# Kernel tuning notes

Measured on AMD Instinct MI355X. Metric: run time of the kernel, lower is better.

The kernel has to match this reference:

```python
import jax, jax.numpy as jnp
import numpy as np

D = 64  # hidden size

def _ffn2(x, w1, b1, w2, b2):
    # Linear -> ReLU -> Linear (no activation after last layer, matching FFN)
    return jax.nn.relu(x @ w1 + b1) @ w2 + b2

def setup_inputs() -> dict:
    key = jax.random.key(0)
    ks = jax.random.split(key, 40)
    B, NP, NY, NO = 512, 128, 1024, 256
    f32 = jnp.float32
    def n(k, sh, s=0.1):
        return (jax.random.normal(k, sh) * s).astype(f32)
    inp = {
        'pred_state': jax.random.normal(ks[0], (B, NP, 2), dtype=f32),
        'prey_state': jax.random.normal(ks[1], (B, NY, 2), dtype=f32),
        'obst_state': jax.random.normal(ks[2], (B, NO, 3), dtype=f32),
        'prey_is_alive': jax.random.randint(ks[3], (B, NY), 0, 2).astype(bool),
        'emb': n(ks[4], (3, D)),
        'e0_w1': n(ks[5], (2, D)), 'e0_b1': n(ks[6], (D,)),
        'e0_w2': n(ks[7], (D, D)), 'e0_b2': n(ks[8], (D,)),
        'e1_w1': n(ks[9], (2, D)), 'e1_b1': n(ks[10], (D,)),
        'e1_w2': n(ks[11], (D, D)), 'e1_b2': n(ks[12], (D,)),
        'e2_w1': n(ks[13], (3, D)), 'e2_b1': n(ks[14], (D,)),
        'e2_w2': n(ks[15], (D, D)), 'e2_b2': n(ks[16], (D,)),
        'wq': n(ks[17], (D, D)), 'bq': n(ks[18], (D,)),
        'wk': n(ks[19], (D, D)), 'bk': n(ks[20], (D,)),
        'wv': n(ks[21], (D, D)), 'bv': n(ks[22], (D,)),
        'wp': n(ks[23], (2, D)), 'bp': n(ks[24], (D,)),
        'wo': n(ks[25], (D, D)), 'bo': n(ks[26], (D,)),
        'n_w1': n(ks[27], (D, D)), 'n_b1': n(ks[28], (D,)),
        'n_w2': n(ks[29], (D, D)), 'n_b2': n(ks[30], (D,)),
        'n_w3': n(ks[31], (D, 1), s=0.01), 'n_b3': n(ks[32], (1,)),
    }
    return inp

def reference(pred_state, prey_state, obst_state, prey_is_alive, emb,
              e0_w1, e0_b1, e0_w2, e0_b2,
              e1_w1, e1_b1, e1_w2, e1_b2,
              e2_w1, e2_b1, e2_w2, e2_b2,
              wq, bq, wk, bk, wv, bv, wp, bp, wo, bo,
              n_w1, n_b1, n_w2, n_b2, n_w3, n_b3):
    # per-entity encoders + type embedding
    x_pred = _ffn2(pred_state, e0_w1, e0_b1, e0_w2, e0_b2) + emb[0]  # [B,NP,D]
    x_prey = _ffn2(prey_state, e1_w1, e1_b1, e1_w2, e1_b2) + emb[1]  # [B,NY,D]
    x_obst = _ffn2(obst_state, e2_w1, e2_b1, e2_w2, e2_b2) + emb[2]  # [B,NO,D]
    x = jnp.concatenate([x_pred, x_prey, x_obst], axis=1)            # [B,N,D]
    pos = jnp.concatenate([pred_state, prey_state, obst_state[..., :2]], axis=1)  # [B,N,2]
    # NOTE: original mask = zeros.unsqueeze(-1) & (...) is identically False -> no masking.
    q = x_pred @ wq + bq   # [B,NP,D]
    k = x @ wk + bk        # [B,N,D]
    v = x @ wv + bv        # [B,N,D]
    # relative positional key bias: pbias = (pos_q - pos_k) @ wp; q . pbias folded as below
    qp = q @ wp.T          # [B,NP,2]
    scale = np.float32(1.0 / np.sqrt(D))
    scores = (jnp.einsum('bqd,bkd->bqk', q, k)
              + jnp.einsum('bqc,bqc->bq', qp, pred_state)[..., None]
              - jnp.einsum('bqc,bkc->bqk', qp, pos)
              + (q @ bp)[..., None]) * scale          # [B,NP,N]
    a = jax.nn.softmax(scores, axis=-1)
    out = jnp.einsum('bqk,bkd->bqd', a, v) @ wo + bo  # [B,NP,D]
    # output FFN with final Tanh
    h = jax.nn.relu(out @ n_w1 + n_b1)
    h = jax.nn.relu(h @ n_w2 + n_b2)
    return jnp.tanh(h @ n_w3 + n_b3)                  # [B,NP,1]
```

## Files before the change

### kernel.cpp

```cpp
#include <hip/hip_runtime.h>
#include <math.h>

#define NB 512
#define NPQ 128
#define NY 1024
#define NO 256
#define NTOT 1408

typedef __attribute__((ext_vector_type(8))) short bf16x8;
typedef __attribute__((ext_vector_type(4))) float f32x4;

__device__ __forceinline__ unsigned short f2bf(float f) {
    unsigned int u = __float_as_uint(f);
    u += 0x7fffu + ((u >> 16) & 1u);
    return (unsigned short)(u >> 16);
}
__device__ __forceinline__ float bf2f(short s) {
    return __uint_as_float(((unsigned int)(unsigned short)s) << 16);
}

union U8  { bf16x8 v; unsigned long long u[2]; };
union U16 { bf16x8 v; uint4 u; };

__global__ __launch_bounds__(256) void k_prep(
    const float* __restrict__ emb,  const float* __restrict__ e0b2,
    const float* __restrict__ e0w2, const float* __restrict__ wq,
    const float* __restrict__ bq,   const float* __restrict__ wk,
    const float* __restrict__ bk,   const float* __restrict__ wp,
    const float* __restrict__ bp,   const float* __restrict__ wvv,
    const float* __restrict__ bv,   const float* __restrict__ wo,
    const float* __restrict__ bo,
    const float* __restrict__ e1b2, const float* __restrict__ e1w2,
    const float* __restrict__ e2b2, const float* __restrict__ e2w2,
    const float* __restrict__ nw1,  const float* __restrict__ nw2,
    float* __restrict__ a0, float* __restrict__ b0g0, float* __restrict__ bvo,
    float* __restrict__ BEP,
    unsigned short* __restrict__ W2P, unsigned short* __restrict__ AqkP,
    unsigned short* __restrict__ P3P, unsigned short* __restrict__ WHP)
{
    const int tid = threadIdx.x;
    __shared__ float sW2q[4096];
    __shared__ float sWvo[4096];
    __shared__ float sAqk[4096];
    __shared__ float sP3[1024];
    __shared__ float scq[64];

    const float* w2s[3] = {e0w2, e1w2, e2w2};
    for (int idx = tid; idx < 1536; idx += 256) {
        const int t = idx >> 9, rem = idx & 511;
        const int mt = rem >> 7, rem2 = rem & 127;
        const int kh = rem2 >> 6, lane = rem2 & 63;
        const int quad = lane >> 4, lq = lane & 15;
        const float* w2 = w2s[t];
        unsigned short v[8];
        #pragma unroll
        for (int j = 0; j < 8; ++j)
            v[j] = f2bf(w2[(kh*32 + quad*8 + j)*64 + mt*16 + lq]);
        *(uint4*)&W2P[(size_t)idx*8] = make_uint4(
            (unsigned int)v[0] | ((unsigned int)v[1] << 16),
            (unsigned int)v[2] | ((unsigned int)v[3] << 16),
            (unsigned int)v[4] | ((unsigned int)v[5] << 16),
            (unsigned int)v[6] | ((unsigned int)v[7] << 16));
    }
    const float* b2s[3] = {e0b2, e1b2, e2b2};
    for (int idx = tid; idx < 192; idx += 256) {
        const int t = idx >> 6, d = idx & 63;
        BEP[idx] = b2s[t][d] + emb[t*64 + d];
    }

    for (int idx = tid; idx < 4096; idx += 256) {
        const int h = idx >> 6, j = idx & 63;
        float s = 0.f;
        for (int e = 0; e < 64; ++e) s += e0w2[h*64+e] * wq[e*64+j];
        sW2q[idx] = s;
    }
    if (tid < 64) {
        const int j = tid;
        float s = bq[j];
        for (int e = 0; e < 64; ++e) s += (e0b2[e] + emb[e]) * wq[e*64+j];
        scq[j] = s;
    }
    for (int idx = tid; idx < 4096; idx += 256) {
        const int e = idx >> 6, o = idx & 63;
        float s = 0.f;
        for (int d = 0; d < 64; ++d) s += wvv[e*64+d] * wo[d*64+o];
        sWvo[idx] = s;
    }
    if (tid < 64) {
        const int o = tid;
        float s = bo[o];
        for (int d = 0; d < 64; ++d) s += bv[d] * wo[d*64+o];
        bvo[o] = s;
    }
    __syncthreads();
    for (int idx = tid; idx < 4096; idx += 256) {
        const int h = idx >> 6, d = idx & 63;
        float s = 0.f;
        for (int j = 0; j < 64; ++j) s += sW2q[h*64+j] * wk[d*64+j];
        sAqk[idx] = s;
    }
    if (tid < 64) {
        const int d = tid;
        float s = 0.f;
        for (int j = 0; j < 64; ++j) s += scq[j] * wk[d*64+j];
        a0[d] = s;
    }
    for (int i = tid; i < 1024; i += 256) {
        const int c = i >> 6, h = i & 63;
        float s = 0.f;
        if (c == 0 || c == 1) {
            for (int j = 0; j < 64; ++j) s += sW2q[h*64+j] * wp[c*64+j];
        } else if (c == 2) {
            for (int j = 0; j < 64; ++j) s += sW2q[h*64+j] * (bp[j] + bk[j]);
        }
        sP3[i] = s;
    }
    if (tid == 0) {
        float s0 = 0.f, s1 = 0.f, s2 = 0.f;
        for (int j = 0; j < 64; ++j) {
            s0 += scq[j] * wp[j];
            s1 += scq[j] * wp[64+j];
            s2 += scq[j] * (bp[j] + bk[j]);
        }
        b0g0[0] = s0; b0g0[1] = s1; b0g0[2] = s2;
    }
    __syncthreads();
    for (int idx = tid; idx < 512; idx += 256) {
        const int fi = idx >> 6, lane = idx & 63;
        const int mt = fi >> 1, kh = fi & 1;
        const int quad = lane >> 4, lq = lane & 15;
        unsigned short v[8];
        #pragma unroll
        for (int j = 0; j < 8; ++j)
            v[j] = f2bf(sAqk[(kh*32 + quad*8 + j)*64 + mt*16 + lq]);
        *(uint4*)&AqkP[(size_t)idx*8] = make_uint4(
            (unsigned int)v[0] | ((unsigned int)v[1] << 16),
            (unsigned int)v[2] | ((unsigned int)v[3] << 16),
            (unsigned int)v[4] | ((unsigned int)v[5] << 16),
            (unsigned int)v[6] | ((unsigned int)v[7] << 16));
    }
    for (int idx = tid; idx < 128; idx += 256) {
        const int kh = idx >> 6, lane = idx & 63;
        const int quad = lane >> 4, lq = lane & 15;
        unsigned short v[8];
        #pragma unroll
        for (int j = 0; j < 8; ++j)
            v[j] = f2bf(sP3[lq*64 + kh*32 + quad*8 + j]);
        *(uint4*)&P3P[(size_t)idx*8] = make_uint4(
            (unsigned int)v[0] | ((unsigned int)v[1] << 16),
            (unsigned int)v[2] | ((unsigned int)v[3] << 16),
            (unsigned int)v[4] | ((unsigned int)v[5] << 16),
            (unsigned int)v[6] | ((unsigned int)v[7] << 16));
    }
    for (int idx = tid; idx < 1536; idx += 256) {
        const int l = idx >> 9, rem = idx & 511;
        const int mt = rem >> 7, rem2 = rem & 127;
        const int kh = rem2 >> 6, lane = rem2 & 63;
        const int quad = lane >> 4, lq = lane & 15;
        unsigned short v[8];
        #pragma unroll
        for (int j = 0; j < 8; ++j) {
            const int off = (kh*32 + quad*8 + j)*64 + mt*16 + lq;
            const float x = (l == 0) ? sWvo[off] : ((l == 1) ? nw1[off] : nw2[off]);
            v[j] = f2bf(x);
        }
        *(uint4*)&WHP[(size_t)idx*8] = make_uint4(
            (unsigned int)v[0] | ((unsigned int)v[1] << 16),
            (unsigned int)v[2] | ((unsigned int)v[3] << 16),
            (unsigned int)v[4] | ((unsigned int)v[5] << 16),
            (unsigned int)v[6] | ((unsigned int)v[7] << 16));
    }
}

__global__ __launch_bounds__(256) void k_encq(
    const float* __restrict__ pred, const float* __restrict__ prey,
    const float* __restrict__ obst,
    const unsigned short* __restrict__ W2P, const float* __restrict__ BEP,
    const float* __restrict__ e0w1, const float* __restrict__ e0b1,
    const float* __restrict__ e1w1, const float* __restrict__ e1b1,
    const float* __restrict__ e2w1, const float* __restrict__ e2b1,
    const unsigned short* __restrict__ AqkP, const float* __restrict__ a0,
    const unsigned short* __restrict__ P3P,  const float* __restrict__ b0g0,
    unsigned short* __restrict__ X, float* __restrict__ POS,
    float* __restrict__ QT, float* __restrict__ QP, float* __restrict__ QC)
{
    const int tid = threadIdx.x, lane = tid & 63, w = tid >> 6;
    const int lq = lane & 15, quad = lane >> 4;
    __shared__ __align__(16) short sH[4][32][68];

    if (blockIdx.x < 1408) {
        const int blk = blockIdx.x;
        int type, lrow0, cin, lsh, nmask, nbase;
        const float *st, *w1, *b1;
        if (blk < 128)       { type=0; lrow0=blk*512;         st=pred; w1=e0w1; b1=e0b1; cin=2; lsh=7;  nmask=NPQ-1; nbase=0; }
        else if (blk < 1152) { type=1; lrow0=(blk-128)*512;   st=prey; w1=e1w1; b1=e1b1; cin=2; lsh=10; nmask=NY-1;  nbase=NPQ; }
        else                 { type=2; lrow0=(blk-1152)*512;  st=obst; w1=e2w1; b1=e2b1; cin=3; lsh=8;  nmask=NO-1;  nbase=NPQ+NY; }

        bf16x8 wfrag[4][2];
        #pragma unroll
        for (int mt = 0; mt < 4; ++mt)
            #pragma unroll
            for (int kh = 0; kh < 2; ++kh)
                wfrag[mt][kh] = *(const bf16x8*)&W2P[(size_t)(((type*4 + mt)*2 + kh)*64 + lane)*8];

        float4 be[4];
        #pragma unroll
        for (int mt = 0; mt < 4; ++mt)
            be[mt] = *(const float4*)&BEP[type*64 + mt*16 + quad*4];

        float b1v[2][8], w0v[2][8], w1v[2][8], w2v[2][8];
        #pragma unroll
        for (int kh = 0; kh < 2; ++kh) {
            const int k0 = kh*32 + quad*8;
            *(float4*)&b1v[kh][0] = *(const float4*)&b1[k0];
            *(float4*)&b1v[kh][4] = *(const float4*)&b1[k0+4];
            *(float4*)&w0v[kh][0] = *(const float4*)&w1[k0];
            *(float4*)&w0v[kh][4] = *(const float4*)&w1[k0+4];
            *(float4*)&w1v[kh][0] = *(const float4*)&w1[64+k0];
            *(float4*)&w1v[kh][4] = *(const float4*)&w1[64+k0+4];
            if (cin == 3) {
                *(float4*)&w2v[kh][0] = *(const float4*)&w1[128+k0];
                *(float4*)&w2v[kh][4] = *(const float4*)&w1[128+k0+4];
            }
        }

        #pragma unroll
        for (int k = 0; k < 4; ++k) {
            const int i = tid*4 + k;
            const int r = i >> 1, c = i & 1;
            const int lr = lrow0 + r;
            const int pb = lr >> lsh, n = nbase + (lr & nmask);
            POS[((size_t)pb*NTOT + n)*2 + c] = st[(size_t)lr*cin + c];
        }

        for (int rt = 0; rt < 8; ++rt) {
            const int lr = lrow0 + w*128 + rt*16 + lq;
            float s0, s1, s2 = 0.f;
            if (cin == 2) {
                const float2 sv = *(const float2*)&st[(size_t)lr*2];
                s0 = sv.x; s1 = sv.y;
            } else {
                const float2 sv = *(const float2*)&st[(size_t)lr*3];
                s0 = sv.x; s1 = sv.y; s2 = st[(size_t)lr*3 + 2];
            }
            bf16x8 hb[2];
            #pragma unroll
            for (int kh = 0; kh < 2; ++kh)
                #pragma unroll
                for (int j = 0; j < 8; ++j) {
                    float a = b1v[kh][j] + s0*w0v[kh][j] + s1*w1v[kh][j];
                    if (cin == 3) a += s2*w2v[kh][j];
                    hb[kh][j] = (short)f2bf(fmaxf(a, 0.f));
                }

            f32x4 acc[4];
            #pragma unroll
            for (int mt = 0; mt < 4; ++mt) acc[mt] = (f32x4){0.f,0.f,0.f,0.f};
            #pragma unroll
            for (int mt = 0; mt < 4; ++mt) {
                acc[mt] = __builtin_amdgcn_mfma_f32_16x16x32_bf16(wfrag[mt][0], hb[0], acc[mt], 0, 0, 0);
                acc[mt] = __builtin_amdgcn_mfma_f32_16x16x32_bf16(wfrag[mt][1], hb[1], acc[mt], 0, 0, 0);
            }

            const int bb = lr >> lsh, n = nbase + (lr & nmask);
            unsigned short* xbase = X + ((size_t)bb*NTOT + n)*64;
            #pragma unroll
            for (int mt = 0; mt < 4; ++mt) {
                const unsigned int u0 = (unsigned int)f2bf(acc[mt][0] + be[mt].x)
                                      | ((unsigned int)f2bf(acc[mt][1] + be[mt].y) << 16);
                const unsigned int u1 = (unsigned int)f2bf(acc[mt][2] + be[mt].z)
                                      | ((unsigned int)f2bf(acc[mt][3] + be[mt].w) << 16);
                *(uint2*)(xbase + mt*16 + quad*4) = make_uint2(u0, u1);
            }
        }
    } else {
        const int b = blockIdx.x - 1408;
        const float w1r0 = e0w1[lane], w1r1 = e0w1[64+lane], b1r = e0b1[lane];
        {
            const float* sp = pred + ((size_t)b*NPQ + w*32)*2;
            #pragma unroll
            for (int r = 0; r < 32; ++r) {
                const float a = b1r + sp[2*r]*w1r0 + sp[2*r+1]*w1r1;
                sH[w][r][lane] = (short)f2bf(fmaxf(a, 0.f));
            }
        }

        bf16x8 wfrag[4][2], a3[2];
        #pragma unroll
        for (int mt = 0; mt < 4; ++mt)
            #pragma unroll
            for (int kh = 0; kh < 2; ++kh)
                wfrag[mt][kh] = *(const bf16x8*)&AqkP[(size_t)((mt*2 + kh)*64 + lane)*8];
        #pragma unroll
        for (int kh = 0; kh < 2; ++kh)
            a3[kh] = *(const bf16x8*)&P3P[(size_t)(kh*64 + lane)*8];

        float4 a0r[4];
        #pragma unroll
        for (int mt = 0; mt < 4; ++mt) a0r[mt] = *(const float4*)&a0[mt*16 + quad*4];
        const float c0 = b0g0[0], c1 = b0g0[1], c2 = b0g0[2];

        __syncthreads();

        for (int bt = 0; bt < 2; ++bt) {
            U8 hb0, hb1;
            const short* hp = &sH[w][bt*16 + lq][0];
            hb0.u[0] = *(const unsigned long long*)(hp + quad*8);
            hb0.u[1] = *(const unsigned long long*)(hp + quad*8 + 4);
            hb1.u[0] = *(const unsigned long long*)(hp + 32 + quad*8);
            hb1.u[1] = *(const unsigned long long*)(hp + 32 + quad*8 + 4);

            f32x4 acc[4], acc3;
            #pragma unroll
            for (int mt = 0; mt < 4; ++mt) acc[mt] = (f32x4){0.f,0.f,0.f,0.f};
            acc3 = (f32x4){0.f,0.f,0.f,0.f};
            #pragma unroll
            for (int mt = 0; mt < 4; ++mt) {
                acc[mt] = __builtin_amdgcn_mfma_f32_16x16x32_bf16(wfrag[mt][0], hb0.v, acc[mt], 0, 0, 0);
                acc[mt] = __builtin_amdgcn_mfma_f32_16x16x32_bf16(wfrag[mt][1], hb1.v, acc[mt], 0, 0, 0);
            }
            acc3 = __builtin_amdgcn_mfma_f32_16x16x32_bf16(a3[0], hb0.v, acc3, 0, 0, 0);
            acc3 = __builtin_amdgcn_mfma_f32_16x16x32_bf16(a3[1], hb1.v, acc3, 0, 0, 0);

            const int row = b*NPQ + w*32 + bt*16 + lq;
            #pragma unroll
            for (int mt = 0; mt < 4; ++mt) {
                *(float4*)&QT[(size_t)row*64 + mt*16 + quad*4] = make_float4(
                    acc[mt][0] + a0r[mt].x, acc[mt][1] + a0r[mt].y,
                    acc[mt][2] + a0r[mt].z, acc[mt][3] + a0r[mt].w);
            }
            if (quad == 0) {
                const float qp0 = acc3[0] + c0, qp1 = acc3[1] + c1, qs = acc3[2] + c2;
                const float p0 = pred[(size_t)row*2], p1 = pred[(size_t)row*2 + 1];
                QP[(size_t)row*2]     = qp0;
                QP[(size_t)row*2 + 1] = qp1;
                QC[row] = qp0*p0 + qp1*p1 + qs;
            }
        }
    }
}

__global__ __launch_bounds__(256, 2) void k_attn(
    const unsigned short* __restrict__ X, const float* __restrict__ POS,
    const float* __restrict__ QT, const float* __restrict__ QP,
    const float* __restrict__ QC, float* __restrict__ OPRE)
{
    const int tid = threadIdx.x, b = blockIdx.x;
    const int w = tid >> 6, lane = tid & 63, lq = lane & 15, quad = lane >> 4;

    __shared__ __align__(16) short sXc[2][64][68];
    __shared__ __align__(16) short sP[4][32][68];

    bf16x8 aq[2][2];
    #pragma unroll
    for (int qt = 0; qt < 2; ++qt) {
        const float* qrow = QT + ((size_t)b*NPQ + w*32 + qt*16 + lq)*64;
        #pragma unroll
        for (int kh = 0; kh < 2; ++kh)
            #pragma unroll
            for (int j = 0; j < 8; ++j)
                aq[qt][kh][j] = (short)f2bf(qrow[kh*32 + quad*8 + j]);
    }

    float qcr[2][4], qp0r[2][4], qp1r[2][4], lacc[2][4];
    f32x4 O[2][4];
    #pragma unroll
    for (int qt = 0; qt < 2; ++qt)
        #pragma unroll
        for (int i = 0; i < 4; ++i) {
            const size_t g = (size_t)b*NPQ + w*32 + qt*16 + quad*4 + i;
            qcr[qt][i]  = QC[g];
            qp0r[qt][i] = -QP[2*g];
            qp1r[qt][i] = -QP[2*g+1];
            lacc[qt][i] = 0.f;
        }
    #pragma unroll
    for (int qt = 0; qt < 2; ++qt)
        #pragma unroll
        for (int nt = 0; nt < 4; ++nt) O[qt][nt] = (f32x4){0.f,0.f,0.f,0.f};
    const float E = 0.180336884f;

    const int skey = tid & 63, sd0 = (tid >> 6) * 16;

    for (int kt = 0; kt < 22; ++kt) {
        const int par = kt & 1;

        const unsigned short* gx = X + ((size_t)b*NTOT + kt*64 + skey)*64 + sd0;
        const uint4 t0 = *(const uint4*)(gx);
        const uint4 t1 = *(const uint4*)(gx + 8);

        if (kt > 0) {
            const int pb = par ^ 1;
            #pragma unroll
            for (int kc = 0; kc < 2; ++kc) {
                U8 pa[2];
                #pragma unroll
                for (int qt = 0; qt < 2; ++qt) {
                    const short* pp = &sP[w][qt*16 + lq][kc*32 + quad*8];
                    pa[qt].u[0] = *(const unsigned long long*)pp;
                    pa[qt].u[1] = *(const unsigned long long*)(pp + 4);
                }
                #pragma unroll
                for (int nt = 0; nt < 4; ++nt) {
                    U8 bv;
                    const short* xp = &sXc[pb][nt*16 + lq][kc*32 + quad*8];
                    bv.u[0] = *(const unsigned long long*)xp;
                    bv.u[1] = *(const unsigned long long*)(xp + 4);
                    O[0][nt] = __builtin_amdgcn_mfma_f32_16x16x32_bf16(pa[0].v, bv.v, O[0][nt], 0, 0, 0);
                    O[1][nt] = __builtin_amdgcn_mfma_f32_16x16x32_bf16(pa[1].v, bv.v, O[1][nt], 0, 0, 0);
                }
            }
        }

        __builtin_amdgcn_sched_barrier(0);

        #pragma unroll
        for (int nt = 0; nt < 4; ++nt) {
            U16 bx0, bx1;
            const unsigned short* xrow = X + ((size_t)b*NTOT + kt*64 + nt*16 + lq)*64;
            bx0.u = *(const uint4*)(xrow + quad*8);
            bx1.u = *(const uint4*)(xrow + 32 + quad*8);
            const float pos0 = POS[((size_t)b*NTOT + kt*64 + nt*16 + lq)*2];
            const float pos1 = POS[((size_t)b*NTOT + kt*64 + nt*16 + lq)*2 + 1];
            #pragma unroll
            for (int qt = 0; qt < 2; ++qt) {
                f32x4 sa = (f32x4){0.f,0.f,0.f,0.f};
                sa = __builtin_amdgcn_mfma_f32_16x16x32_bf16(aq[qt][0], bx0.v, sa, 0, 0, 0);
                sa = __builtin_amdgcn_mfma_f32_16x16x32_bf16(aq[qt][1], bx1.v, sa, 0, 0, 0);
                #pragma unroll
                for (int i = 0; i < 4; ++i) {
                    float s = sa[i] + qcr[qt][i];
                    s = fmaf(qp0r[qt][i], pos0, s);
                    s = fmaf(qp1r[qt][i], pos1, s);
                    const float p = exp2f(s * E);
                    lacc[qt][i] += p;
                    sP[w][qt*16 + quad*4 + i][nt*16 + lq] = (short)f2bf(p);
                }
            }
        }

        {
            unsigned short tmp[16];
            *(uint4*)tmp = t0; *(uint4*)(tmp+8) = t1;
            #pragma unroll
            for (int j = 0; j < 16; ++j) sXc[par][sd0+j][skey] = (short)tmp[j];
        }

        __syncthreads();
    }

    {
        #pragma unroll
        for (int kc = 0; kc < 2; ++kc) {
            U8 pa[2];
            #pragma unroll
            for (int qt = 0; qt < 2; ++qt) {
                const short* pp = &sP[w][qt*16 + lq][kc*32 + quad*8];
                pa[qt].u[0] = *(const unsigned long long*)pp;
                pa[qt].u[1] = *(const unsigned long long*)(pp + 4);
            }
            #pragma unroll
            for (int nt = 0; nt < 4; ++nt) {
                U8 bv;
                const short* xp = &sXc[1][nt*16 + lq][kc*32 + quad*8];
                bv.u[0] = *(const unsigned long long*)xp;
                bv.u[1] = *(const unsigned long long*)(xp + 4);
                O[0][nt] = __builtin_amdgcn_mfma_f32_16x16x32_bf16(pa[0].v, bv.v, O[0][nt], 0, 0, 0);
                O[1][nt] = __builtin_amdgcn_mfma_f32_16x16x32_bf16(pa[1].v, bv.v, O[1][nt], 0, 0, 0);
            }
        }
    }

    #pragma unroll
    for (int qt = 0; qt < 2; ++qt)
        #pragma unroll
        for (int i = 0; i < 4; ++i) {
            #pragma unroll
            for (int off = 1; off < 16; off <<= 1)
                lacc[qt][i] += __shfl_xor(lacc[qt][i], off);
            const float rl = 1.f / lacc[qt][i];
            float* orow = OPRE + ((size_t)b*NPQ + w*32 + qt*16 + quad*4 + i)*64;
            #pragma unroll
            for (int nt = 0; nt < 4; ++nt) orow[nt*16 + lq] = O[qt][nt][i] * rl;
        }
}

__global__ __launch_bounds__(256) void k_head(
    const float* __restrict__ OPRE,
    const unsigned short* __restrict__ WHP,
    const float* __restrict__ bvo, const float* __restrict__ nb1,
    const float* __restrict__ nb2,
    const float* __restrict__ nw3, const float* __restrict__ nb3,
    float* __restrict__ OUT)
{
    const int tid = threadIdx.x, b = blockIdx.x;
    const int w = tid >> 6, lane = tid & 63, lq = lane & 15, quad = lane >> 4;
    __shared__ __align__(16) short sA[128][68];
    __shared__ __align__(16) short sB[128][68];
    __shared__ float sw3[64];

    for (int i = tid*4; i < 8192; i += 1024) {
        const float4 v = *(const float4*)&OPRE[(size_t)b*8192 + i];
        const int r = i >> 6, d = i & 63;
        const unsigned int u0 = (unsigned int)f2bf(v.x) | ((unsigned int)f2bf(v.y) << 16);
        const unsigned int u1 = (unsigned int)f2bf(v.z) | ((unsigned int)f2bf(v.w) << 16);
        *(uint2*)&sA[r][d] = make_uint2(u0, u1);
    }
    if (tid < 64) sw3[tid] = nw3[tid];
    __syncthreads();

    const float* Bs[3] = {bvo, nb1, nb2};
    for (int l = 0; l < 3; ++l) {
        bf16x8 wfrag[4][2];
        #pragma unroll
        for (int mt = 0; mt < 4; ++mt)
            #pragma unroll
            for (int kh = 0; kh < 2; ++kh)
                wfrag[mt][kh] = *(const bf16x8*)&WHP[(size_t)(((l*4 + mt)*2 + kh)*64 + lane)*8];
        const float* Bb = Bs[l];
        float be[4][4];
        #pragma unroll
        for (int mt = 0; mt < 4; ++mt)
            #pragma unroll
            for (int i = 0; i < 4; ++i) be[mt][i] = Bb[mt*16 + quad*4 + i];

        short (*src)[68] = (l & 1) ? sB : sA;
        short (*dst)[68] = (l & 1) ? sA : sB;
        const bool doRelu = (l >= 1);

        for (int bt = 0; bt < 2; ++bt) {
            U8 hb0, hb1;
            const short* hp = &src[w*32 + bt*16 + lq][0];
            hb0.u[0] = *(const unsigned long long*)(hp + quad*8);
            hb0.u[1] = *(const unsigned long long*)(hp + quad*8 + 4);
            hb1.u[0] = *(const unsigned long long*)(hp + 32 + quad*8);
            hb1.u[1] = *(const unsigned long long*)(hp + 32 + quad*8 + 4);

            f32x4 acc[4];
            #pragma unroll
            for (int mt = 0; mt < 4; ++mt) acc[mt] = (f32x4){0.f,0.f,0.f,0.f};
            #pragma unroll
            for (int mt = 0; mt < 4; ++mt) {
                acc[mt] = __builtin_amdgcn_mfma_f32_16x16x32_bf16(wfrag[mt][0], hb0.v, acc[mt], 0, 0, 0);
                acc[mt] = __builtin_amdgcn_mfma_f32_16x16x32_bf16(wfrag[mt][1], hb1.v, acc[mt], 0, 0, 0);
            }
            const int row = w*32 + bt*16 + lq;
            #pragma unroll
            for (int mt = 0; mt < 4; ++mt) {
                float v0 = acc[mt][0] + be[mt][0];
                float v1 = acc[mt][1] + be[mt][1];
                float v2 = acc[mt][2] + be[mt][2];
                float v3 = acc[mt][3] + be[mt][3];
                if (doRelu) {
                    v0 = fmaxf(v0, 0.f); v1 = fmaxf(v1, 0.f);
                    v2 = fmaxf(v2, 0.f); v3 = fmaxf(v3, 0.f);
                }
                const unsigned int u0 = (unsigned int)f2bf(v0) | ((unsigned int)f2bf(v1) << 16);
                const unsigned int u1 = (unsigned int)f2bf(v2) | ((unsigned int)f2bf(v3) << 16);
                *(uint2*)&dst[row][mt*16 + quad*4] = make_uint2(u0, u1);
            }
        }
        __syncthreads();
    }

    if (tid < 128) {
        const int row = tid;
        float acc = nb3[0];
        #pragma unroll 16
        for (int d = 0; d < 64; ++d) acc += bf2f(sB[row][d]) * sw3[d];
        OUT[(size_t)b*NPQ + row] = tanhf(acc);
    }
}

extern "C" void kernel_launch(void* const* d_in, const int* in_sizes, int n_in,
                              void* d_out, int out_size, void* d_ws, size_t ws_size,
                              hipStream_t stream)
{
    const float* pred = (const float*)d_in[0];
    const float* prey = (const float*)d_in[1];
    const float* obst = (const float*)d_in[2];
    const float* emb  = (const float*)d_in[4];
    const float* e0w1 = (const float*)d_in[5];
    const float* e0b1 = (const float*)d_in[6];
    const float* e0w2 = (const float*)d_in[7];
    const float* e0b2 = (const float*)d_in[8];
    const float* e1w1 = (const float*)d_in[9];
    const float* e1b1 = (const float*)d_in[10];
    const float* e1w2 = (const float*)d_in[11];
    const float* e1b2 = (const float*)d_in[12];
    const float* e2w1 = (const float*)d_in[13];
    const float* e2b1 = (const float*)d_in[14];
    const float* e2w2 = (const float*)d_in[15];
    const float* e2b2 = (const float*)d_in[16];
    const float* wq  = (const float*)d_in[17];
    const float* bq  = (const float*)d_in[18];
    const float* wk  = (const float*)d_in[19];
    const float* bk  = (const float*)d_in[20];
    const float* wvv = (const float*)d_in[21];
    const float* bv  = (const float*)d_in[22];
    const float* wp  = (const float*)d_in[23];
    const float* bp  = (const float*)d_in[24];
    const float* wo  = (const float*)d_in[25];
    const float* bo  = (const float*)d_in[26];
    const float* nw1 = (const float*)d_in[27];
    const float* nb1 = (const float*)d_in[28];
    const float* nw2 = (const float*)d_in[29];
    const float* nb2 = (const float*)d_in[30];
    const float* nw3 = (const float*)d_in[31];
    const float* nb3 = (const float*)d_in[32];

    char* ws = (char*)d_ws;
    unsigned short* X = (unsigned short*)ws;
    float* F    = (float*)(ws + 92274688);
    float* POS  = F;
    float* QT   = POS + 1441792;
    float* QP   = QT  + 4194304;
    float* QC   = QP  + 131072;
    float* OPRE = QC  + 65536;
    float* a0   = OPRE + 4194304;
    float* b0g0 = a0  + 64;
    float* bvo  = b0g0 + 4;
    float* BEP  = bvo + 64;
    unsigned short* W2P  = (unsigned short*)(BEP + 192);
    unsigned short* AqkP = W2P + 12288;
    unsigned short* P3P  = AqkP + 4096;
    unsigned short* WHP  = P3P + 1024;

    k_prep<<<1, 256, 0, stream>>>(emb, e0b2, e0w2, wq, bq, wk, bk, wp, bp,
        wvv, bv, wo, bo, e1b2, e1w2, e2b2, e2w2, nw1, nw2,
        a0, b0g0, bvo, BEP, W2P, AqkP, P3P, WHP);
    k_encq<<<1920, 256, 0, stream>>>(pred, prey, obst, W2P, BEP,
        e0w1, e0b1, e1w1, e1b1, e2w1, e2b1,
        AqkP, a0, P3P, b0g0, X, POS, QT, QP, QC);
    k_attn<<<512, 256, 0, stream>>>(X, POS, QT, QP, QC, OPRE);
    k_head<<<512, 256, 0, stream>>>(OPRE, WHP, bvo, nb1, nb2,
        nw3, nb3, (float*)d_out);
}
```

Baseline: 303.7 us.

## Split single-block weight prep kernel into two multi-block kernels

The one-block preprocessing kernel, which folds weight matrices (W2·Wq, Wv·Wo, Aqk, P3) and packs them into bf16 MFMA layouts, is split into two launches. The first runs 43 blocks and the second runs 4, with intermediate fused matrices staged in global workspace instead of shared memory. This spreads the serial 64x64x64 matrix products across many compute units and adds multiple accumulators to shorten dependency chains. It costs one extra kernel launch and a global-memory round trip for the intermediates.

Measured after the change: 256.3 us. 15.6% less time.

```diff
diff --git a/kernel.cpp b/kernel.cpp
--- a/kernel.cpp
+++ b/kernel.cpp
@@ -22,153 +22,216 @@
 union U8  { bf16x8 v; unsigned long long u[2]; };
 union U16 { bf16x8 v; uint4 u; };
 
-__global__ __launch_bounds__(256) void k_prep(
+__global__ __launch_bounds__(256) void k_prepA(
     const float* __restrict__ emb,  const float* __restrict__ e0b2,
     const float* __restrict__ e0w2, const float* __restrict__ wq,
-    const float* __restrict__ bq,   const float* __restrict__ wk,
-    const float* __restrict__ bk,   const float* __restrict__ wp,
-    const float* __restrict__ bp,   const float* __restrict__ wvv,
-    const float* __restrict__ bv,   const float* __restrict__ wo,
-    const float* __restrict__ bo,
+    const float* __restrict__ bq,   const float* __restrict__ wp,
+    const float* __restrict__ bp,   const float* __restrict__ bk,
+    const float* __restrict__ wvv,  const float* __restrict__ bv,
+    const float* __restrict__ wo,   const float* __restrict__ bo,
     const float* __restrict__ e1b2, const float* __restrict__ e1w2,
     const float* __restrict__ e2b2, const float* __restrict__ e2w2,
     const float* __restrict__ nw1,  const float* __restrict__ nw2,
-    float* __restrict__ a0, float* __restrict__ b0g0, float* __restrict__ bvo,
-    float* __restrict__ BEP,
-    unsigned short* __restrict__ W2P, unsigned short* __restrict__ AqkP,
-    unsigned short* __restrict__ P3P, unsigned short* __restrict__ WHP)
+    float* __restrict__ W2qG, float* __restrict__ WvoG,
+    float* __restrict__ scqG, float* __restrict__ b0g0,
+    float* __restrict__ bvo,  float* __restrict__ BEP,
+    unsigned short* __restrict__ W2P, unsigned short* __restrict__ WHP)
 {
-    const int tid = threadIdx.x;
-    __shared__ float sW2q[4096];
-    __shared__ float sWvo[4096];
-    __shared__ float sAqk[4096];
-    __shared__ float sP3[1024];
-    __shared__ float scq[64];
-
-    const float* w2s[3] = {e0w2, e1w2, e2w2};
-    for (int idx = tid; idx < 1536; idx += 256) {
-        const int t = idx >> 9, rem = idx & 511;
+    const int tid = threadIdx.x, blk = blockIdx.x;
+
+    if (blk < 16) {
+        const int idx = blk*256 + tid;
+        const int h = idx >> 6, j = idx & 63;
+        float s0 = 0.f, s1 = 0.f, s2 = 0.f, s3 = 0.f;
+        #pragma unroll 4
+        for (int e = 0; e < 64; e += 4) {
+            s0 = fmaf(e0w2[h*64+e],   wq[(e  )*64+j], s0);
+            s1 = fmaf(e0w2[h*64+e+1], wq[(e+1)*64+j], s1);
+            s2 = fmaf(e0w2[h*64+e+2], wq[(e+2)*64+j], s2);
+            s3 = fmaf(e0w2[h*64+e+3], wq[(e+3)*64+j], s3);
+        }
+        W2qG[idx] = (s0 + s1) + (s2 + s3);
+    } else if (blk < 32) {
+        const int idx = (blk-16)*256 + tid;
+        const int e = idx >> 6, o = idx & 63;
+        float s0 = 0.f, s1 = 0.f, s2 = 0.f, s3 = 0.f;
+        #pragma unroll 4
+        for (int d = 0; d < 64; d += 4) {
+            s0 = fmaf(wvv[e*64+d],   wo[(d  )*64+o], s0);
+            s1 = fmaf(wvv[e*64+d+1], wo[(d+1)*64+o], s1);
+            s2 = fmaf(wvv[e*64+d+2], wo[(d+2)*64+o], s2);
+            s3 = fmaf(wvv[e*64+d+3], wo[(d+3)*64+o], s3);
+        }
+        WvoG[idx] = (s0 + s1) + (s2 + s3);
+    } else if (blk < 38) {
+        const int idx = (blk-32)*256 + tid;
+        if (idx < 1536) {
+            const int t = idx >> 9, rem = idx & 511;
+            const int mt = rem >> 7, rem2 = rem & 127;
+            const int kh = rem2 >> 6, lane = rem2 & 63;
+            const int quad = lane >> 4, lq = lane & 15;
+            const float* w2 = (t == 0) ? e0w2 : ((t == 1) ? e1w2 : e2w2);
+            unsigned short v[8];
+            #pragma unroll
+            for (int j = 0; j < 8; ++j)
+                v[j] = f2bf(w2[(kh*32 + quad*8 + j)*64 + mt*16 + lq]);
+            *(uint4*)&W2P[(size_t)idx*8] = make_uint4(
+                (unsigned int)v[0] | ((unsigned int)v[1] << 16),
+                (unsigned int)v[2] | ((unsigned int)v[3] << 16),
+                (unsigned int)v[4] | ((unsigned int)v[5] << 16),
+                (unsigned int)v[6] | ((unsigned int)v[7] << 16));
+        }
+    } else if (blk < 42) {
+        const int idx = 512 + (blk-38)*256 + tid;
+        const int l = idx >> 9, rem = idx & 511;
         const int mt = rem >> 7, rem2 = rem & 127;
         const int kh = rem2 >> 6, lane = rem2 & 63;
         const int quad = lane >> 4, lq = lane & 15;
-        const float* w2 = w2s[t];
+        const float* W = (l == 1) ? nw1 : nw2;
         unsigned short v[8];
         #pragma unroll
         for (int j = 0; j < 8; ++j)
-            v[j] = f2bf(w2[(kh*32 + quad*8 + j)*64 + mt*16 + lq]);
-        *(uint4*)&W2P[(size_t)idx*8] = make_uint4(
+            v[j] = f2bf(W[(kh*32 + quad*8 + j)*64 + mt*16 + lq]);
+        *(uint4*)&WHP[(size_t)idx*8] = make_uint4(
             (unsigned int)v[0] | ((unsigned int)v[1] << 16),
             (unsigned int)v[2] | ((unsigned int)v[3] << 16),
             (unsigned int)v[4] | ((unsigned int)v[5] << 16),
             (unsigned int)v[6] | ((unsigned int)v[7] << 16));
-    }
-    const float* b2s[3] = {e0b2, e1b2, e2b2};
-    for (int idx = tid; idx < 192; idx += 256) {
-        const int t = idx >> 6, d = idx & 63;
-        BEP[idx] = b2s[t][d] + emb[t*64 + d];
-    }
-
-    for (int idx = tid; idx < 4096; idx += 256) {
-        const int h = idx >> 6, j = idx & 63;
-        float s = 0.f;
-        for (int e = 0; e < 64; ++e) s += e0w2[h*64+e] * wq[e*64+j];
-        sW2q[idx] = s;
-    }
-    if (tid < 64) {
-        const int j = tid;
-        float s = bq[j];
-        for (int e = 0; e < 64; ++e) s += (e0b2[e] + emb[e]) * wq[e*64+j];
-        scq[j] = s;
-    }
-    for (int idx = tid; idx < 4096; idx += 256) {
-        const int e = idx >> 6, o = idx & 63;
-        float s = 0.f;
-        for (int d = 0; d < 64; ++d) s += wvv[e*64+d] * wo[d*64+o];
-        sWvo[idx] = s;
-    }
-    if (tid < 64) {
-        const int o = tid;
-        float s = bo[o];
-        for (int d = 0; d < 64; ++d) s += bv[d] * wo[d*64+o];
-        bvo[o] = s;
-    }
-    __syncthreads();
-    for (int idx = tid; idx < 4096; idx += 256) {
-        const int h = idx >> 6, d = idx & 63;
-        float s = 0.f;
-        for (int j = 0; j < 64; ++j) s += sW2q[h*64+j] * wk[d*64+j];
-        sAqk[idx] = s;
-    }
-    if (tid < 64) {
-        const int d = tid;
-        float s = 0.f;
-        for (int j = 0; j < 64; ++j) s += scq[j] * wk[d*64+j];
-        a0[d] = s;
-    }
-    for (int i = tid; i < 1024; i += 256) {
-        const int c = i >> 6, h = i & 63;
-        float s = 0.f;
-        if (c == 0 || c == 1) {
-            for (int j = 0; j < 64; ++j) s += sW2q[h*64+j] * wp[c*64+j];
-        } else if (c == 2) {
-            for (int j = 0; j < 64; ++j) s += sW2q[h*64+j] * (bp[j] + bk[j]);
-        }
-        sP3[i] = s;
-    }
-    if (tid == 0) {
-        float s0 = 0.f, s1 = 0.f, s2 = 0.f;
-        for (int j = 0; j < 64; ++j) {
-            s0 += scq[j] * wp[j];
-            s1 += scq[j] * wp[64+j];
-            s2 += scq[j] * (bp[j] + bk[j]);
-        }
-        b0g0[0] = s0; b0g0[1] = s1; b0g0[2] = s2;
-    }
-    __syncthreads();
-    for (int idx = tid; idx < 512; idx += 256) {
+    } else {
+        __shared__ float scq[64];
+        if (tid < 64) {
+            const int j = tid;
+            float s = bq[j];
+            for (int e = 0; e < 64; ++e) s += (e0b2[e] + emb[e]) * wq[e*64+j];
+            scq[j] = s;
+            scqG[j] = s;
+        }
+        if (tid >= 64 && tid < 128) {
+            const int o = tid - 64;
+            float s = bo[o];
+            for (int d = 0; d < 64; ++d) s += bv[d] * wo[d*64+o];
+            bvo[o] = s;
+        }
+        {
+            const int i = tid - 64;
+            if (i >= 64 && i < 256) {
+                const int idx = i - 64;
+                const int t = idx >> 6, d = idx & 63;
+                const float* b2 = (t == 0) ? e0b2 : ((t == 1) ? e1b2 : e2b2);
+                BEP[idx] = b2[d] + emb[t*64 + d];
+            }
+        }
+        __syncthreads();
+        if (tid == 0) {
+            float s0 = 0.f, s1 = 0.f, s2 = 0.f;
+            for (int j = 0; j < 64; ++j) {
+                s0 += scq[j] * wp[j];
+                s1 += scq[j] * wp[64+j];
+                s2 += scq[j] * (bp[j] + bk[j]);
+            }
+            b0g0[0] = s0; b0g0[1] = s1; b0g0[2] = s2;
+        }
+    }
+}
+
+__global__ __launch_bounds__(256) void k_prepB(
+    const float* __restrict__ W2qG, const float* __restrict__ WvoG,
+    const float* __restrict__ scqG,
+    const float* __restrict__ wk, const float* __restrict__ wp,
+    const float* __restrict__ bp, const float* __restrict__ bk,
+    unsigned short* __restrict__ AqkP, unsigned short* __restrict__ P3P,
+    float* __restrict__ a0, unsigned short* __restrict__ WHP)
+{
+    const int tid = threadIdx.x, blk = blockIdx.x;
+
+    if (blk < 2) {
+        const int idx = blk*256 + tid;
         const int fi = idx >> 6, lane = idx & 63;
         const int mt = fi >> 1, kh = fi & 1;
         const int quad = lane >> 4, lq = lane & 15;
+        const int d = mt*16 + lq;
         unsigned short v[8];
         #pragma unroll
-        for (int j = 0; j < 8; ++j)
-            v[j] = f2bf(sAqk[(kh*32 + quad*8 + j)*64 + mt*16 + lq]);
+        for (int jj = 0; jj < 8; ++jj) {
+            const int h = kh*32 + quad*8 + jj;
+            float s0 = 0.f, s1 = 0.f, s2 = 0.f, s3 = 0.f;
+            #pragma unroll 4
+            for (int j = 0; j < 64; j += 4) {
+                const float4 a = *(const float4*)&W2qG[h*64 + j];
+                const float4 b = *(const float4*)&wk[d*64 + j];
+                s0 = fmaf(a.x, b.x, s0); s1 = fmaf(a.y, b.y, s1);
+                s2 = fmaf(a.z, b.z, s2); s3 = fmaf(a.w, b.w, s3);
+            }
+            v[jj] = f2bf((s0 + s1) + (s2 + s3));
+        }
         *(uint4*)&AqkP[(size_t)idx*8] = make_uint4(
             (unsigned int)v[0] | ((unsigned int)v[1] << 16),
             (unsigned int)v[2] | ((unsigned int)v[3] << 16),
             (unsigned int)v[4] | ((unsigned int)v[5] << 16),
             (unsigned int)v[6] | ((unsigned int)v[7] << 16));
-    }
-    for (int idx = tid; idx < 128; idx += 256) {
-        const int kh = idx >> 6, lane = idx & 63;
-        const int quad = lane >> 4, lq = lane & 15;
-        unsigned short v[8];
-        #pragma unroll
-        for (int j = 0; j < 8; ++j)
-            v[j] = f2bf(sP3[lq*64 + kh*32 + quad*8 + j]);
-        *(uint4*)&P3P[(size_t)idx*8] = make_uint4(
-            (unsigned int)v[0] | ((unsigned int)v[1] << 16),
-            (unsigned int)v[2] | ((unsigned int)v[3] << 16),
-            (unsigned int)v[4] | ((unsigned int)v[5] << 16),
-            (unsigned int)v[6] | ((unsigned int)v[7] << 16));
-    }
-    for (int idx = tid; idx < 1536; idx += 256) {
-        const int l = idx >> 9, rem = idx & 511;
-        const int mt = rem >> 7, rem2 = rem & 127;
-        const int kh = rem2 >> 6, lane = rem2 & 63;
-        const int quad = lane >> 4, lq = lane & 15;
-        unsigned short v[8];
-        #pragma unroll
-        for (int j = 0; j < 8; ++j) {
-            const int off = (kh*32 + quad*8 + j)*64 + mt*16 + lq;
-            const float x = (l == 0) ? sWvo[off] : ((l == 1) ? nw1[off] : nw2[off]);
-            v[j] = f2bf(x);
-        }
-        *(uint4*)&WHP[(size_t)idx*8] = make_uint4(
-            (unsigned int)v[0] | ((unsigned int)v[1] << 16),
-            (unsigned int)v[2] | ((unsigned int)v[3] << 16),
-            (unsigned int)v[4] | ((unsigned int)v[5] << 16),
-            (unsigned int)v[6] | ((unsigned int)v[7] << 16));
+    } else if (blk == 2) {
+        if (tid < 128) {
+            const int idx = tid;
+            const int kh = idx >> 6, lane = idx & 63;
+            const int quad = lane >> 4, lq = lane & 15;
+            unsigned short v[8];
+            #pragma unroll
+            for (int jj = 0; jj < 8; ++jj) {
+                const int h = kh*32 + quad*8 + jj;
+                float val = 0.f;
+                if (lq == 0 || lq == 1) {
+                    float s0 = 0.f, s1 = 0.f;
+                    #pragma unroll 8
+                    for (int j = 0; j < 64; j += 2) {
+                        s0 = fmaf(W2qG[h*64+j],   wp[lq*64+j],   s0);
+                        s1 = fmaf(W2qG[h*64+j+1], wp[lq*64+j+1], s1);
+                    }
+                    val = s0 + s1;
+                } else if (lq == 2) {
+                    float s0 = 0.f, s1 = 0.f;
+                    #pragma unroll 8
+                    for (int j = 0; j < 64; j += 2) {
+                        s0 = fmaf(W2qG[h*64+j],   bp[j]   + bk[j],   s0);
+                        s1 = fmaf(W2qG[h*64+j+1], bp[j+1] + bk[j+1], s1);
+                    }
+                    val = s0 + s1;
+                }
+                v[jj] = f2bf(val);
+            }
+            *(uint4*)&P3P[(size_t)idx*8] = make_uint4(
+                (unsigned int)v[0] | ((unsigned int)v[1] << 16),
+                (unsigned int)v[2] | ((unsigned int)v[3] << 16),
+                (unsigned int)v[4] | ((unsigned int)v[5] << 16),
+                (unsigned int)v[6] | ((unsigned int)v[7] << 16));
+        } else if (tid < 192) {
+            const int d = tid - 128;
+            float s0 = 0.f, s1 = 0.f, s2 = 0.f, s3 = 0.f;
+            #pragma unroll 4
+            for (int j = 0; j < 64; j += 4) {
+                const float4 a = *(const float4*)&scqG[j];
+                const float4 b = *(const float4*)&wk[d*64 + j];
+                s0 = fmaf(a.x, b.x, s0); s1 = fmaf(a.y, b.y, s1);
+                s2 = fmaf(a.z, b.z, s2); s3 = fmaf(a.w, b.w, s3);
+            }
+            a0[d] = (s0 + s1) + (s2 + s3);
+        }
+    } else {
+        #pragma unroll
+        for (int pass = 0; pass < 2; ++pass) {
+            const int idx = pass*256 + tid;
+            const int mt = idx >> 7, rem2 = idx & 127;
+            const int kh = rem2 >> 6, lane = rem2 & 63;
+            const int quad = lane >> 4, lq = lane & 15;
+            unsigned short v[8];
+            #pragma unroll
+            for (int j = 0; j < 8; ++j)
+                v[j] = f2bf(WvoG[(kh*32 + quad*8 + j)*64 + mt*16 + lq]);
+            *(uint4*)&WHP[(size_t)idx*8] = make_uint4(
+                (unsigned int)v[0] | ((unsigned int)v[1] << 16),
+                (unsigned int)v[2] | ((unsigned int)v[3] << 16),
+                (unsigned int)v[4] | ((unsigned int)v[5] << 16),
+                (unsigned int)v[6] | ((unsigned int)v[7] << 16));
+        }
     }
 }
 
@@ -621,14 +684,19 @@
     float* b0g0 = a0  + 64;
     float* bvo  = b0g0 + 4;
     float* BEP  = bvo + 64;
-    unsigned short* W2P  = (unsigned short*)(BEP + 192);
+    float* W2qG = BEP + 192;
+    float* WvoG = W2qG + 4096;
+    float* scqG = WvoG + 4096;
+    unsigned short* W2P  = (unsigned short*)(scqG + 64);
     unsigned short* AqkP = W2P + 12288;
     unsigned short* P3P  = AqkP + 4096;
     unsigned short* WHP  = P3P + 1024;
 
-    k_prep<<<1, 256, 0, stream>>>(emb, e0b2, e0w2, wq, bq, wk, bk, wp, bp,
+    k_prepA<<<43, 256, 0, stream>>>(emb, e0b2, e0w2, wq, bq, wp, bp, bk,
         wvv, bv, wo, bo, e1b2, e1w2, e2b2, e2w2, nw1, nw2,
-        a0, b0g0, bvo, BEP, W2P, AqkP, P3P, WHP);
+        W2qG, WvoG, scqG, b0g0, bvo, BEP, W2P, WHP);
+    k_prepB<<<4, 256, 0, stream>>>(W2qG, WvoG, scqG, wk, wp, bp, bk,
+        AqkP, P3P, a0, WHP);
     k_encq<<<1920, 256, 0, stream>>>(pred, prey, obst, W2P, BEP,
         e0w1, e0b1, e1w1, e1b1, e2w1, e2b1,
         AqkP, a0, P3P, b0g0, X, POS, QT, QP, QC);
```
